# Optimization experiments

Hardware: AMD Instinct MI355X
Metric: run time of the kernel (lower is better)

The kernel has to match this reference:

```python
import jax, jax.numpy as jnp
import numpy as np

N_RADIAL = 5
N_BASIS = 7
R_MAX = 6.0
R_MIN = 0.5
N_SPECIES = 119
N_ATOMS = 50000
N_EDGES = 1000000


def tril_2d_indices(n):
    return np.array([(i, j) for i in range(n) for j in range(i + 1)], dtype=np.int32)


def tril_3d_indices(n):
    return np.array([(i, j, k) for i in range(n) for j in range(i + 1) for k in range(j + 1)], dtype=np.int32)


TRIL2 = tril_2d_indices(N_RADIAL)  # [15, 2]
TRIL3 = tril_3d_indices(N_RADIAL)  # [35, 3]


def setup_inputs() -> dict:
    key = jax.random.key(0)
    k1, k2, k3, k4 = jax.random.split(key, 4)
    R = jax.random.normal(k1, (N_ATOMS, 3), dtype=jnp.float32) * 1.5
    Z = jax.random.randint(k2, (N_ATOMS,), 0, N_SPECIES, dtype=jnp.int32)
    neighbor_idxs = jax.random.randint(k3, (2, N_EDGES), 0, N_ATOMS, dtype=jnp.int32)
    box = jnp.zeros((3,), dtype=jnp.float32)
    W = jax.random.normal(k4, (N_SPECIES, N_SPECIES, N_RADIAL, N_BASIS), dtype=jnp.float32)
    return {"R": R, "Z": Z, "neighbor_idxs": neighbor_idxs, "box": box, "W": W}


def reference(R, Z, neighbor_idxs, box, W):
    n_atoms = R.shape[0]
    idx_i, idx_j = neighbor_idxs[0], neighbor_idxs[1]
    # free-space displacement (init_box == 0): R[idx_j] - R[idx_i]
    dr_vec = (R[idx_j] - R[idx_i]).astype(jnp.float32)  # [E, 3]
    dr = jnp.sqrt(jnp.sum(dr_vec * dr_vec, axis=-1))    # [E]
    dn = dr_vec / (dr + 1e-5)[:, None]                  # unit directions [E, 3]

    # radial function: Gaussian basis * cosine cutoff, species-pair coefficients
    shifts = R_MIN + (R_MAX - R_MIN) / N_BASIS * jnp.arange(N_BASIS, dtype=jnp.float32)
    betta = float(N_BASIS ** 2) / float(R_MAX ** 2)
    rad_norm = float((2.0 * betta / np.pi) ** 0.25)
    basis = rad_norm * jnp.exp(-betta * (dr[:, None] - shifts) ** 2)  # [E, n_basis]
    cutoff = 0.5 * (jnp.cos(np.pi * dr / R_MAX) + 1.0) * (dr < R_MAX).astype(dr.dtype)
    coeffs = W[Z[idx_i], Z[idx_j]]  # [E, n_radial, n_basis]
    embed_norm = float(1.0 / np.sqrt(N_BASIS))
    radial = jnp.einsum('en,ern->er', basis, coeffs) * cutoff[:, None] * embed_norm  # [E, R]

    # mask padded (self-index) neighbors
    radial = radial * (idx_i != idx_j).astype(radial.dtype)[:, None]

    # geometric moments: scatter-add per-edge rank-0..3 outer products onto atoms
    seg = lambda x: jax.ops.segment_sum(x, idx_j, num_segments=n_atoms)
    m0 = seg(radial)                                           # [A, R]
    m1 = seg(radial[:, :, None] * dn[:, None, :])              # [A, R, 3]
    dn2 = dn[:, None, :, None] * dn[:, None, None, :]          # [E, 1, 3, 3]
    m2 = seg(radial[:, :, None, None] * dn2)                   # [A, R, 3, 3]
    dn3 = dn2[..., None] * dn[:, None, None, None, :]          # [E, 1, 3, 3, 3]
    m3 = seg(radial[:, :, None, None, None] * dn3)             # [A, R, 3, 3, 3]

    contr_0 = m0
    contr_1 = jnp.einsum('ari,asi->rsa', m1, m1)
    contr_2 = jnp.einsum('arij,asij->rsa', m2, m2)
    contr_3 = jnp.einsum('arijk,asijk->rsa', m3, m3)
    contr_4 = jnp.einsum('arij,asik,atjk->rsta', m2, m2, m2)
    contr_5 = jnp.einsum('ari,asj,atij->rsta', m1, m1, m2)
    contr_6 = jnp.einsum('arijk,asijl,atkl->rsta', m3, m3, m2)
    contr_7 = jnp.einsum('arijk,asij,atk->rsta', m3, m2, m1)

    i2, j2 = TRIL2[:, 0], TRIL2[:, 1]
    i3, j3, k3 = TRIL3[:, 0], TRIL3[:, 1], TRIL3[:, 2]
    n_symm01 = TRIL2.shape[0] * N_RADIAL  # 75

    c1 = jnp.transpose(contr_1[i2, j2])                                    # [A, 15]
    c2 = jnp.transpose(contr_2[i2, j2])                                    # [A, 15]
    c3 = jnp.transpose(contr_3[i2, j2])                                    # [A, 15]
    c4 = jnp.transpose(contr_4[i3, j3, k3])                                # [A, 35]
    c5 = jnp.transpose(jnp.reshape(contr_5[i2, j2], (n_symm01, -1)))       # [A, 75]
    c6 = jnp.transpose(jnp.reshape(contr_6[i2, j2], (n_symm01, -1)))       # [A, 75]
    c7 = jnp.transpose(jnp.reshape(contr_7, (N_RADIAL ** 3, -1)))          # [A, 125]

    return jnp.concatenate([contr_0, c1, c2, c3, c4, c5, c6, c7], axis=-1)  # [A, 360]
```

## Files before the change

### kernel.cpp

```cpp
#include <hip/hip_runtime.h>
#include <cstdint>
#include <cstddef>

#define CAP 64
#define NSP 119
#define CPAD 16

__device__ constexpr int IDX2[9]  = {0,1,2, 1,3,4, 2,4,5};
__device__ constexpr int IDX3[27] = {0,1,2, 1,3,4, 2,4,5,
                                     1,3,4, 3,6,7, 4,7,8,
                                     2,4,5, 4,7,8, 5,8,9};
__device__ constexpr int PR2[15] = {0,1,1,2,2,2,3,3,3,3,4,4,4,4,4};
__device__ constexpr int PS2[15] = {0,0,1,0,1,2,0,1,2,3,0,1,2,3,4};
__device__ constexpr int CB4[15] = {50,51,52,54,55,57,60,61,63,66,70,71,73,76,80};

__global__ __launch_bounds__(256) void rz_pack_kernel(
    const float* __restrict__ R, const int* __restrict__ Z,
    float4* __restrict__ RZ, int n_atoms)
{
    int t = blockIdx.x * blockDim.x + threadIdx.x;
    if (t >= n_atoms) return;
    RZ[t] = make_float4(R[3*t], R[3*t+1], R[3*t+2], __int_as_float(Z[t]));
}

__global__ __launch_bounds__(256) void pad_w_kernel(
    const float* __restrict__ W, float* __restrict__ Wp, int n_el)
{
    int t = blockIdx.x * blockDim.x + threadIdx.x;
    if (t >= n_el) return;
    int rc = t / 36;
    int u  = t - rc * 36;
    Wp[t] = (u < 35) ? W[rc * 35 + u] : 0.f;
}

__device__ __forceinline__ bool edge_math(
    float4 rzi, float4 rzj, const float4* __restrict__ Wp4,
    float rv[5], float dn[3])
{
    float dx = rzj.x - rzi.x, dy = rzj.y - rzi.y, dz = rzj.z - rzi.z;
    float dr = sqrtf(dx*dx + dy*dy + dz*dz);
    if (!(dr < 6.0f)) return false;

    float inv = 1.0f / (dr + 1e-5f);
    dn[0] = dx*inv; dn[1] = dy*inv; dn[2] = dz*inv;

    const float betta      = 49.0f/36.0f;
    const float rad_norm   = 0.96481270f;
    const float embed_norm = 0.37796447f;
    const float PI_F       = 3.14159265358979f;
    float cut = 0.5f * (__cosf(PI_F * dr * (1.0f/6.0f)) + 1.0f) * rad_norm * embed_norm;

    float basis[7];
    #pragma unroll
    for (int n = 0; n < 7; n++) {
        float d = dr - (0.5f + (5.5f/7.0f) * (float)n);
        basis[n] = __expf(-betta * d * d);
    }

    int zi = __float_as_int(rzi.w);
    int zj = __float_as_int(rzj.w);
    int base4 = (zi * NSP + zj) * 9;

    float rad[5] = {0,0,0,0,0};
    #pragma unroll
    for (int q = 0; q < 9; q++) {
        float4 wq = Wp4[base4 + q];
        #pragma unroll
        for (int c = 0; c < 4; c++) {
            int f = 4*q + c;
            if (f < 35) {
                float wv = (c==0) ? wq.x : (c==1) ? wq.y : (c==2) ? wq.z : wq.w;
                rad[f/7] += basis[f%7] * wv;
            }
        }
    }
    #pragma unroll
    for (int r = 0; r < 5; r++) rv[r] = rad[r] * cut;
    return true;
}

__global__ __launch_bounds__(256) void edge_compute_kernel(
    const int* __restrict__ nbr, const float4* __restrict__ RZ,
    const float4* __restrict__ Wp4,
    int* __restrict__ cnt, int* __restrict__ binsIdx,
    float4* __restrict__ edgeF, int n_edges)
{
    int e = blockIdx.x * blockDim.x + threadIdx.x;
    if (e >= n_edges) return;
    int i = nbr[e];
    int j = nbr[n_edges + e];
    if (i == j) return;
    float4 rzi = RZ[i];
    float4 rzj = RZ[j];
    float rv[5], dn[3];
    if (!edge_math(rzi, rzj, Wp4, rv, dn)) return;

    int pos = atomicAdd(&cnt[j * CPAD], 1);
    if (pos < CAP) {
        binsIdx[(size_t)j * CAP + pos] = e;
        edgeF[2*(size_t)e + 0] = make_float4(rv[0], rv[1], rv[2], rv[3]);
        edgeF[2*(size_t)e + 1] = make_float4(rv[4], dn[0], dn[1], dn[2]);
    }
}

__global__ __launch_bounds__(256) void scatter_bins_kernel(
    const int* __restrict__ nbr, int* __restrict__ cnt,
    int* __restrict__ bins, int n_edges)
{
    int e = blockIdx.x * blockDim.x + threadIdx.x;
    if (e >= n_edges) return;
    int i = nbr[e];
    int j = nbr[n_edges + e];
    if (i == j) return;
    int pos = atomicAdd(&cnt[j], 1);
    if (pos < CAP) bins[(size_t)j * CAP + pos] = i;
}

__device__ __forceinline__ void c6_range(const float* m, float* o, int plo, int phi) {
    for (int p = plo; p < phi; p++) {
        int r = PR2[p], s = PS2[p];
        const float* m3r = m + 50 + r * 10;
        const float* m3s = m + 50 + s * 10;
        float A[3][3] = {{0,0,0},{0,0,0},{0,0,0}};
        #pragma unroll
        for (int i = 0; i < 3; i++)
            #pragma unroll
            for (int j = 0; j < 3; j++)
                #pragma unroll
                for (int k = 0; k < 3; k++)
                    #pragma unroll
                    for (int l = 0; l < 3; l++)
                        A[k][l] += m3r[IDX3[(i*3+j)*3+k]] * m3s[IDX3[(i*3+j)*3+l]];
        int col = 160 + p * 5;
        for (int t = 0; t < 5; t++) {
            const float* m2t = m + 20 + t * 6;
            float acc = 0.f;
            #pragma unroll
            for (int k = 0; k < 3; k++)
                #pragma unroll
                for (int l = 0; l < 3; l++)
                    acc += A[k][l] * m2t[IDX2[k*3+l]];
            o[col + t] = acc;
        }
    }
}

__device__ __forceinline__ void c4_range(const float* m, float* o, int plo, int phi) {
    for (int p = plo; p < phi; p++) {
        int r = PR2[p], s = PS2[p];
        const float* m2r = m + 20 + r * 6;
        const float* m2s = m + 20 + s * 6;
        float B[3][3] = {{0,0,0},{0,0,0},{0,0,0}};
        #pragma unroll
        for (int i = 0; i < 3; i++)
            #pragma unroll
            for (int j = 0; j < 3; j++)
                #pragma unroll
                for (int k = 0; k < 3; k++)
                    B[j][k] += m2r[IDX2[i*3+j]] * m2s[IDX2[i*3+k]];
        int col = CB4[p];
        for (int t = 0; t <= s; t++) {
            const float* m2t = m + 20 + t * 6;
            float acc = 0.f;
            #pragma unroll
            for (int j = 0; j < 3; j++)
                #pragma unroll
                for (int k = 0; k < 3; k++)
                    acc += B[j][k] * m2t[IDX2[j*3+k]];
            o[col + t] = acc;
        }
    }
}

__device__ __forceinline__ void c5_range(const float* m, float* o, int plo, int phi) {
    for (int p = plo; p < phi; p++) {
        int r = PR2[p], s = PS2[p];
        const float* m1r = m + 5 + r * 3;
        const float* m1s = m + 5 + s * 3;
        float P[3][3];
        #pragma unroll
        for (int i = 0; i < 3; i++)
            #pragma unroll
            for (int j = 0; j < 3; j++)
                P[i][j] = m1r[i] * m1s[j];
        int col = 85 + p * 5;
        for (int t = 0; t < 5; t++) {
            const float* m2t = m + 20 + t * 6;
            float acc = 0.f;
            #pragma unroll
            for (int i = 0; i < 3; i++)
                #pragma unroll
                for (int j = 0; j < 3; j++)
                    acc += P[i][j] * m2t[IDX2[i*3+j]];
            o[col + t] = acc;
        }
    }
}

__device__ __forceinline__ void c7_all(const float* m, float* o) {
    for (int r = 0; r < 5; r++) {
        const float* m3r = m + 50 + r * 10;
        for (int s = 0; s < 5; s++) {
            const float* m2s = m + 20 + s * 6;
            float v[3] = {0,0,0};
            #pragma unroll
            for (int i = 0; i < 3; i++)
                #pragma unroll
                for (int j = 0; j < 3; j++)
                    #pragma unroll
                    for (int k = 0; k < 3; k++)
                        v[k] += m3r[IDX3[(i*3+j)*3+k]] * m2s[IDX2[i*3+j]];
            int col = 235 + (r * 5 + s) * 5;
            for (int t = 0; t < 5; t++) {
                const float* m1t = m + 5 + t * 3;
                o[col + t] = v[0]*m1t[0] + v[1]*m1t[1] + v[2]*m1t[2];
            }
        }
    }
}

__device__ __forceinline__ void c0123(const float* m, float* o) {
    for (int r = 0; r < 5; r++) o[r] = m[r];
    const float W2[6]  = {1,2,2,1,2,1};
    const float W3[10] = {1,3,3,3,6,3,1,3,3,1};
    int c1 = 5, c2 = 20, c3 = 35;
    for (int r = 0; r < 5; r++) {
        const float* a1r = m + 5 + r * 3;
        const float* a2r = m + 20 + r * 6;
        const float* a3r = m + 50 + r * 10;
        for (int s = 0; s <= r; s++) {
            const float* a1s = m + 5 + s * 3;
            const float* a2s = m + 20 + s * 6;
            const float* a3s = m + 50 + s * 10;
            float d1 = 0.f, d2 = 0.f, d3 = 0.f;
            #pragma unroll
            for (int u = 0; u < 3; u++)  d1 += a1r[u] * a1s[u];
            #pragma unroll
            for (int u = 0; u < 6; u++)  d2 += W2[u] * a2r[u] * a2s[u];
            #pragma unroll
            for (int u = 0; u < 10; u++) d3 += W3[u] * a3r[u] * a3s[u];
            o[c1++] = d1; o[c2++] = d2; o[c3++] = d3;
        }
    }
}

__device__ __forceinline__ void moments_to_out(
    float acc[100], float sm[64][101], int tid, int a0, int n_atoms,
    float* __restrict__ out)
{
    #pragma unroll
    for (int u = 0; u < 100; u++) {
        acc[u] += __shfl_xor(acc[u], 1);
        acc[u] += __shfl_xor(acc[u], 2);
    }
    int g  = tid >> 2;
    int l4 = tid & 3;
    if (a0 + g < n_atoms && l4 == 0) {
        #pragma unroll
        for (int u = 0; u < 100; u++) sm[g][u] = acc[u];
    }
    __syncthreads();

    int lane = tid & 63;
    int w    = tid >> 6;
    int aa   = a0 + lane;
    if (aa < n_atoms) {
        const float* m = sm[lane];
        float* o = out + (size_t)aa * 360;
        if (w == 0) {
            c6_range(m, o, 0, 10);
        } else if (w == 1) {
            c6_range(m, o, 10, 15);
            c4_range(m, o, 0, 7);
        } else if (w == 2) {
            c4_range(m, o, 7, 15);
            c5_range(m, o, 0, 15);
        } else {
            c7_all(m, o);
            c0123(m, o);
        }
    }
}

__global__ __launch_bounds__(256) void accum_payload_kernel(
    const int* __restrict__ cnt, const int* __restrict__ binsIdx,
    const float4* __restrict__ edgeF,
    float* __restrict__ out, int n_atoms)
{
    __shared__ float sm[64][101];
    int tid = threadIdx.x;
    int a0  = blockIdx.x * 64;
    int g   = tid >> 2;
    int l4  = tid & 3;
    int a   = a0 + g;

    float acc[100];
    #pragma unroll
    for (int u = 0; u < 100; u++) acc[u] = 0.f;

    if (a < n_atoms) {
        int cn = cnt[a * CPAD]; if (cn > CAP) cn = CAP;
        const int* row = binsIdx + (size_t)a * CAP;
        for (int es = l4; es < cn; es += 4) {
            int e = row[es];
            float4 q0 = edgeF[2*(size_t)e + 0];
            float4 q1 = edgeF[2*(size_t)e + 1];
            float rv[5] = {q0.x, q0.y, q0.z, q0.w, q1.x};
            float dn1[3] = {q1.y, q1.z, q1.w};
            float p2[6] = {dn1[0]*dn1[0], dn1[0]*dn1[1], dn1[0]*dn1[2],
                           dn1[1]*dn1[1], dn1[1]*dn1[2], dn1[2]*dn1[2]};
            float p3[10] = {p2[0]*dn1[0], p2[0]*dn1[1], p2[0]*dn1[2],
                            p2[1]*dn1[1], p2[1]*dn1[2], p2[2]*dn1[2],
                            p2[3]*dn1[1], p2[3]*dn1[2], p2[4]*dn1[2],
                            p2[5]*dn1[2]};
            #pragma unroll
            for (int r = 0; r < 5; r++) {
                float rvv = rv[r];
                acc[r] += rvv;
                #pragma unroll
                for (int u = 0; u < 3; u++)  acc[5  + r*3  + u] += rvv * dn1[u];
                #pragma unroll
                for (int u = 0; u < 6; u++)  acc[20 + r*6  + u] += rvv * p2[u];
                #pragma unroll
                for (int u = 0; u < 10; u++) acc[50 + r*10 + u] += rvv * p3[u];
            }
        }
    }
    moments_to_out(acc, sm, tid, a0, n_atoms, out);
}

__global__ __launch_bounds__(256) void accum_gather_kernel(
    const float4* __restrict__ RZ, const float4* __restrict__ Wp4,
    const int* __restrict__ cnt, const int* __restrict__ bins,
    float* __restrict__ out, int n_atoms)
{
    __shared__ float sm[64][101];
    int tid = threadIdx.x;
    int a0  = blockIdx.x * 64;
    int g   = tid >> 2;
    int l4  = tid & 3;
    int a   = a0 + g;

    float acc[100];
    #pragma unroll
    for (int u = 0; u < 100; u++) acc[u] = 0.f;

    if (a < n_atoms) {
        int cn = cnt[a]; if (cn > CAP) cn = CAP;
        float4 rza = RZ[a];
        for (int e = l4; e < cn; e += 4) {
            int i = bins[(size_t)a * CAP + e];
            float4 rzi = RZ[i];
            float rv[5], dn1[3];
            if (!edge_math(rzi, rza, Wp4, rv, dn1)) continue;
            float p2[6] = {dn1[0]*dn1[0], dn1[0]*dn1[1], dn1[0]*dn1[2],
                           dn1[1]*dn1[1], dn1[1]*dn1[2], dn1[2]*dn1[2]};
            float p3[10] = {p2[0]*dn1[0], p2[0]*dn1[1], p2[0]*dn1[2],
                            p2[1]*dn1[1], p2[1]*dn1[2], p2[2]*dn1[2],
                            p2[3]*dn1[1], p2[3]*dn1[2], p2[4]*dn1[2],
                            p2[5]*dn1[2]};
            #pragma unroll
            for (int r = 0; r < 5; r++) {
                float rvv = rv[r];
                acc[r] += rvv;
                #pragma unroll
                for (int u = 0; u < 3; u++)  acc[5  + r*3  + u] += rvv * dn1[u];
                #pragma unroll
                for (int u = 0; u < 6; u++)  acc[20 + r*6  + u] += rvv * p2[u];
                #pragma unroll
                for (int u = 0; u < 10; u++) acc[50 + r*10 + u] += rvv * p3[u];
            }
        }
    }
    moments_to_out(acc, sm, tid, a0, n_atoms, out);
}

extern "C" void kernel_launch(void* const* d_in, const int* in_sizes, int n_in,
                              void* d_out, int out_size, void* d_ws, size_t ws_size,
                              hipStream_t stream)
{
    const float* R   = (const float*)d_in[0];
    const int*   Z   = (const int*)d_in[1];
    const int*   nbr = (const int*)d_in[2];
    const float* W   = (const float*)d_in[4];
    float* out = (float*)d_out;

    int n_atoms = in_sizes[0] / 3;
    int n_edges = in_sizes[2] / 2;
    int n_wel   = NSP * NSP * 36;

    char* ws = (char*)d_ws;

    size_t szCntPad = (size_t)n_atoms * CPAD * 4;
    size_t szIdx    = (size_t)n_atoms * CAP * 4;
    size_t szEdgeF  = (size_t)n_edges * 32;
    size_t szRZ     = (size_t)n_atoms * 16;
    size_t szWp     = (size_t)n_wel * 4;
    size_t needP    = szCntPad + szIdx + szEdgeF + szRZ + szWp;

    if (ws_size >= needP) {
        int*    cnt     = (int*)ws;
        int*    binsIdx = (int*)(ws + szCntPad);
        float4* edgeF   = (float4*)(ws + szCntPad + szIdx);
        float4* RZ      = (float4*)(ws + szCntPad + szIdx + szEdgeF);
        float4* Wp4     = (float4*)(ws + szCntPad + szIdx + szEdgeF + szRZ);

        hipMemsetAsync(cnt, 0, szCntPad, stream);
        rz_pack_kernel<<<(n_atoms + 255)/256, 256, 0, stream>>>(R, Z, RZ, n_atoms);
        pad_w_kernel<<<(n_wel + 255)/256, 256, 0, stream>>>(W, (float*)Wp4, n_wel);
        edge_compute_kernel<<<(n_edges + 255)/256, 256, 0, stream>>>(
            nbr, RZ, Wp4, cnt, binsIdx, edgeF, n_edges);
        accum_payload_kernel<<<(n_atoms + 63)/64, 256, 0, stream>>>(
            cnt, binsIdx, edgeF, out, n_atoms);
    } else {
        int*    cnt  = (int*)ws;
        int*    bins = (int*)(ws + 204800);
        float4* RZ   = (float4*)(ws + 204800 + szIdx);
        float4* Wp4  = (float4*)(ws + 204800 + szIdx + szRZ);

        hipMemsetAsync(cnt, 0, (size_t)n_atoms * 4, stream);
        rz_pack_kernel<<<(n_atoms + 255)/256, 256, 0, stream>>>(R, Z, RZ, n_atoms);
        pad_w_kernel<<<(n_wel + 255)/256, 256, 0, stream>>>(W, (float*)Wp4, n_wel);
        scatter_bins_kernel<<<(n_edges + 255)/256, 256, 0, stream>>>(nbr, cnt, bins, n_edges);
        accum_gather_kernel<<<(n_atoms + 63)/64, 256, 0, stream>>>(
            RZ, Wp4, cnt, bins, out, n_atoms);
    }
}
```

Baseline: 135.9 us.

## Transpose edge bins and map atoms to lanes with LDS atomic reduction

Bin indices are now stored slot-major (pos * n_atoms + j), so that in the accumulate kernel consecutive lanes read consecutive atoms and the index loads coalesce. Each atom is now handled by one lane per wave, with the four waves splitting its edges, in place of four adjacent lanes splitting them. Partial moments are combined with shared-memory atomicAdd in place of xor shuffles, which needs an LDS zero-fill and an extra barrier. The risk is 100 LDS atomics per thread, more lane divergence from uneven per-atom edge counts, and scattered writes from the edge kernel into the transposed layout.

```diff
diff --git a/kernel.cpp b/kernel.cpp
--- a/kernel.cpp
+++ b/kernel.cpp
@@ -82,8 +82,8 @@
 __global__ __launch_bounds__(256) void edge_compute_kernel(
     const int* __restrict__ nbr, const float4* __restrict__ RZ,
     const float4* __restrict__ Wp4,
-    int* __restrict__ cnt, int* __restrict__ binsIdx,
-    float4* __restrict__ edgeF, int n_edges)
+    int* __restrict__ cnt, int* __restrict__ binsIdxT,
+    float4* __restrict__ edgeF, int n_edges, int n_atoms)
 {
     int e = blockIdx.x * blockDim.x + threadIdx.x;
     if (e >= n_edges) return;
@@ -97,7 +97,7 @@
 
     int pos = atomicAdd(&cnt[j * CPAD], 1);
     if (pos < CAP) {
-        binsIdx[(size_t)j * CAP + pos] = e;
+        binsIdxT[(size_t)pos * n_atoms + j] = e;
         edgeF[2*(size_t)e + 0] = make_float4(rv[0], rv[1], rv[2], rv[3]);
         edgeF[2*(size_t)e + 1] = make_float4(rv[4], dn[0], dn[1], dn[2]);
     }
@@ -244,26 +244,10 @@
     }
 }
 
-__device__ __forceinline__ void moments_to_out(
-    float acc[100], float sm[64][101], int tid, int a0, int n_atoms,
-    float* __restrict__ out)
-{
-    #pragma unroll
-    for (int u = 0; u < 100; u++) {
-        acc[u] += __shfl_xor(acc[u], 1);
-        acc[u] += __shfl_xor(acc[u], 2);
-    }
-    int g  = tid >> 2;
-    int l4 = tid & 3;
-    if (a0 + g < n_atoms && l4 == 0) {
-        #pragma unroll
-        for (int u = 0; u < 100; u++) sm[g][u] = acc[u];
-    }
-    __syncthreads();
-
-    int lane = tid & 63;
-    int w    = tid >> 6;
-    int aa   = a0 + lane;
+__device__ __forceinline__ void contract_4wave(
+    float sm[64][101], int lane, int w, int a0, int n_atoms, float* __restrict__ out)
+{
+    int aa = a0 + lane;
     if (aa < n_atoms) {
         const float* m = sm[lane];
         float* o = out + (size_t)aa * 360;
@@ -282,17 +266,21 @@
     }
 }
 
-__global__ __launch_bounds__(256) void accum_payload_kernel(
-    const int* __restrict__ cnt, const int* __restrict__ binsIdx,
+__global__ __launch_bounds__(256) void accum_contract_kernel(
+    const int* __restrict__ cnt, const int* __restrict__ binsIdxT,
     const float4* __restrict__ edgeF,
     float* __restrict__ out, int n_atoms)
 {
     __shared__ float sm[64][101];
-    int tid = threadIdx.x;
-    int a0  = blockIdx.x * 64;
-    int g   = tid >> 2;
-    int l4  = tid & 3;
-    int a   = a0 + g;
+    int tid  = threadIdx.x;
+    int lane = tid & 63;
+    int w    = tid >> 6;
+    int a0   = blockIdx.x * 64;
+    int a    = a0 + lane;
+
+    float* smf = &sm[0][0];
+    for (int t = tid; t < 64*101; t += 256) smf[t] = 0.f;
+    __syncthreads();
 
     float acc[100];
     #pragma unroll
@@ -300,12 +288,11 @@
 
     if (a < n_atoms) {
         int cn = cnt[a * CPAD]; if (cn > CAP) cn = CAP;
-        const int* row = binsIdx + (size_t)a * CAP;
-        for (int es = l4; es < cn; es += 4) {
-            int e = row[es];
+        for (int k = w; k < cn; k += 4) {
+            int e = binsIdxT[(size_t)k * n_atoms + a];
             float4 q0 = edgeF[2*(size_t)e + 0];
             float4 q1 = edgeF[2*(size_t)e + 1];
-            float rv[5] = {q0.x, q0.y, q0.z, q0.w, q1.x};
+            float rv[5]  = {q0.x, q0.y, q0.z, q0.w, q1.x};
             float dn1[3] = {q1.y, q1.z, q1.w};
             float p2[6] = {dn1[0]*dn1[0], dn1[0]*dn1[1], dn1[0]*dn1[2],
                            dn1[1]*dn1[1], dn1[1]*dn1[2], dn1[2]*dn1[2]};
@@ -325,8 +312,12 @@
                 for (int u = 0; u < 10; u++) acc[50 + r*10 + u] += rvv * p3[u];
             }
         }
-    }
-    moments_to_out(acc, sm, tid, a0, n_atoms, out);
+        #pragma unroll
+        for (int u = 0; u < 100; u++) atomicAdd(&sm[lane][u], acc[u]);
+    }
+    __syncthreads();
+
+    contract_4wave(sm, lane, w, a0, n_atoms, out);
 }
 
 __global__ __launch_bounds__(256) void accum_gather_kernel(
@@ -372,7 +363,19 @@
             }
         }
     }
-    moments_to_out(acc, sm, tid, a0, n_atoms, out);
+
+    #pragma unroll
+    for (int u = 0; u < 100; u++) {
+        acc[u] += __shfl_xor(acc[u], 1);
+        acc[u] += __shfl_xor(acc[u], 2);
+    }
+    if (a < n_atoms && l4 == 0) {
+        #pragma unroll
+        for (int u = 0; u < 100; u++) sm[g][u] = acc[u];
+    }
+    __syncthreads();
+
+    contract_4wave(sm, tid & 63, tid >> 6, a0, n_atoms, out);
 }
 
 extern "C" void kernel_launch(void* const* d_in, const int* in_sizes, int n_in,
@@ -399,19 +402,19 @@
     size_t needP    = szCntPad + szIdx + szEdgeF + szRZ + szWp;
 
     if (ws_size >= needP) {
-        int*    cnt     = (int*)ws;
-        int*    binsIdx = (int*)(ws + szCntPad);
-        float4* edgeF   = (float4*)(ws + szCntPad + szIdx);
-        float4* RZ      = (float4*)(ws + szCntPad + szIdx + szEdgeF);
-        float4* Wp4     = (float4*)(ws + szCntPad + szIdx + szEdgeF + szRZ);
+        int*    cnt      = (int*)ws;
+        int*    binsIdxT = (int*)(ws + szCntPad);
+        float4* edgeF    = (float4*)(ws + szCntPad + szIdx);
+        float4* RZ       = (float4*)(ws + szCntPad + szIdx + szEdgeF);
+        float4* Wp4      = (float4*)(ws + szCntPad + szIdx + szEdgeF + szRZ);
 
         hipMemsetAsync(cnt, 0, szCntPad, stream);
         rz_pack_kernel<<<(n_atoms + 255)/256, 256, 0, stream>>>(R, Z, RZ, n_atoms);
         pad_w_kernel<<<(n_wel + 255)/256, 256, 0, stream>>>(W, (float*)Wp4, n_wel);
         edge_compute_kernel<<<(n_edges + 255)/256, 256, 0, stream>>>(
-            nbr, RZ, Wp4, cnt, binsIdx, edgeF, n_edges);
-        accum_payload_kernel<<<(n_atoms + 63)/64, 256, 0, stream>>>(
-            cnt, binsIdx, edgeF, out, n_atoms);
+            nbr, RZ, Wp4, cnt, binsIdxT, edgeF, n_edges, n_atoms);
+        accum_contract_kernel<<<(n_atoms + 63)/64, 256, 0, stream>>>(
+            cnt, binsIdxT, edgeF, out, n_atoms);
     } else {
         int*    cnt  = (int*)ws;
         int*    bins = (int*)(ws + 204800);
```

Result: slower. 243.9 us (+79.4%).

## Write edge payloads directly into per-atom slots instead of index indirection

Applied to the files above, without the earlier changes.

Adds a new path used when workspace is large enough: the edge kernel writes its computed radial and direction payload straight into the destination atom's bin slot instead of storing an edge index plus a separate per-edge payload array. The accumulation kernel then reads contiguous per-atom slot rows, which removes the index load and the random gather over edge payloads. In exchange, the edge kernel's writes become scattered, the workspace grows to atoms*CAP*32 bytes, and the new path only runs if the harness provides that much workspace. The shared accumulation code is also factored into helpers.

```diff
diff --git a/kernel.cpp b/kernel.cpp
--- a/kernel.cpp
+++ b/kernel.cpp
@@ -79,7 +79,30 @@
     return true;
 }
 
-__global__ __launch_bounds__(256) void edge_compute_kernel(
+__global__ __launch_bounds__(256) void edge_compute_slot_kernel(
+    const int* __restrict__ nbr, const float4* __restrict__ RZ,
+    const float4* __restrict__ Wp4,
+    int* __restrict__ cnt, float4* __restrict__ pay, int n_edges)
+{
+    int e = blockIdx.x * blockDim.x + threadIdx.x;
+    if (e >= n_edges) return;
+    int i = nbr[e];
+    int j = nbr[n_edges + e];
+    if (i == j) return;
+    float4 rzi = RZ[i];
+    float4 rzj = RZ[j];
+    float rv[5], dn[3];
+    if (!edge_math(rzi, rzj, Wp4, rv, dn)) return;
+
+    int pos = atomicAdd(&cnt[j * CPAD], 1);
+    if (pos < CAP) {
+        size_t slot = ((size_t)j * CAP + pos) * 2;
+        pay[slot + 0] = make_float4(rv[0], rv[1], rv[2], rv[3]);
+        pay[slot + 1] = make_float4(rv[4], dn[0], dn[1], dn[2]);
+    }
+}
+
+__global__ __launch_bounds__(256) void edge_compute_r4_kernel(
     const int* __restrict__ nbr, const float4* __restrict__ RZ,
     const float4* __restrict__ Wp4,
     int* __restrict__ cnt, int* __restrict__ binsIdx,
@@ -244,26 +267,10 @@
     }
 }
 
-__device__ __forceinline__ void moments_to_out(
-    float acc[100], float sm[64][101], int tid, int a0, int n_atoms,
-    float* __restrict__ out)
-{
-    #pragma unroll
-    for (int u = 0; u < 100; u++) {
-        acc[u] += __shfl_xor(acc[u], 1);
-        acc[u] += __shfl_xor(acc[u], 2);
-    }
-    int g  = tid >> 2;
-    int l4 = tid & 3;
-    if (a0 + g < n_atoms && l4 == 0) {
-        #pragma unroll
-        for (int u = 0; u < 100; u++) sm[g][u] = acc[u];
-    }
-    __syncthreads();
-
-    int lane = tid & 63;
-    int w    = tid >> 6;
-    int aa   = a0 + lane;
+__device__ __forceinline__ void contract_4wave(
+    float sm[64][101], int lane, int w, int a0, int n_atoms, float* __restrict__ out)
+{
+    int aa = a0 + lane;
     if (aa < n_atoms) {
         const float* m = sm[lane];
         float* o = out + (size_t)aa * 360;
@@ -282,7 +289,76 @@
     }
 }
 
-__global__ __launch_bounds__(256) void accum_payload_kernel(
+__device__ __forceinline__ void moments_to_out(
+    float acc[100], float sm[64][101], int tid, int a0, int n_atoms,
+    float* __restrict__ out)
+{
+    #pragma unroll
+    for (int u = 0; u < 100; u++) {
+        acc[u] += __shfl_xor(acc[u], 1);
+        acc[u] += __shfl_xor(acc[u], 2);
+    }
+    int g  = tid >> 2;
+    int l4 = tid & 3;
+    if (a0 + g < n_atoms && l4 == 0) {
+        #pragma unroll
+        for (int u = 0; u < 100; u++) sm[g][u] = acc[u];
+    }
+    __syncthreads();
+    contract_4wave(sm, tid & 63, tid >> 6, a0, n_atoms, out);
+}
+
+__device__ __forceinline__ void accum_edge(float acc[100], float4 q0, float4 q1)
+{
+    float rv[5]  = {q0.x, q0.y, q0.z, q0.w, q1.x};
+    float dn1[3] = {q1.y, q1.z, q1.w};
+    float p2[6] = {dn1[0]*dn1[0], dn1[0]*dn1[1], dn1[0]*dn1[2],
+                   dn1[1]*dn1[1], dn1[1]*dn1[2], dn1[2]*dn1[2]};
+    float p3[10] = {p2[0]*dn1[0], p2[0]*dn1[1], p2[0]*dn1[2],
+                    p2[1]*dn1[1], p2[1]*dn1[2], p2[2]*dn1[2],
+                    p2[3]*dn1[1], p2[3]*dn1[2], p2[4]*dn1[2],
+                    p2[5]*dn1[2]};
+    #pragma unroll
+    for (int r = 0; r < 5; r++) {
+        float rvv = rv[r];
+        acc[r] += rvv;
+        #pragma unroll
+        for (int u = 0; u < 3; u++)  acc[5  + r*3  + u] += rvv * dn1[u];
+        #pragma unroll
+        for (int u = 0; u < 6; u++)  acc[20 + r*6  + u] += rvv * p2[u];
+        #pragma unroll
+        for (int u = 0; u < 10; u++) acc[50 + r*10 + u] += rvv * p3[u];
+    }
+}
+
+__global__ __launch_bounds__(256) void accum_slot_kernel(
+    const int* __restrict__ cnt, const float4* __restrict__ pay,
+    float* __restrict__ out, int n_atoms)
+{
+    __shared__ float sm[64][101];
+    int tid = threadIdx.x;
+    int a0  = blockIdx.x * 64;
+    int g   = tid >> 2;
+    int l4  = tid & 3;
+    int a   = a0 + g;
+
+    float acc[100];
+    #pragma unroll
+    for (int u = 0; u < 100; u++) acc[u] = 0.f;
+
+    if (a < n_atoms) {
+        int cn = cnt[a * CPAD]; if (cn > CAP) cn = CAP;
+        const float4* row = pay + (size_t)a * CAP * 2;
+        for (int es = l4; es < cn; es += 4) {
+            float4 q0 = row[2*es + 0];
+            float4 q1 = row[2*es + 1];
+            accum_edge(acc, q0, q1);
+        }
+    }
+    moments_to_out(acc, sm, tid, a0, n_atoms, out);
+}
+
+__global__ __launch_bounds__(256) void accum_payload_r4_kernel(
     const int* __restrict__ cnt, const int* __restrict__ binsIdx,
     const float4* __restrict__ edgeF,
     float* __restrict__ out, int n_atoms)
@@ -305,25 +381,7 @@
             int e = row[es];
             float4 q0 = edgeF[2*(size_t)e + 0];
             float4 q1 = edgeF[2*(size_t)e + 1];
-            float rv[5] = {q0.x, q0.y, q0.z, q0.w, q1.x};
-            float dn1[3] = {q1.y, q1.z, q1.w};
-            float p2[6] = {dn1[0]*dn1[0], dn1[0]*dn1[1], dn1[0]*dn1[2],
-                           dn1[1]*dn1[1], dn1[1]*dn1[2], dn1[2]*dn1[2]};
-            float p3[10] = {p2[0]*dn1[0], p2[0]*dn1[1], p2[0]*dn1[2],
-                            p2[1]*dn1[1], p2[1]*dn1[2], p2[2]*dn1[2],
-                            p2[3]*dn1[1], p2[3]*dn1[2], p2[4]*dn1[2],
-                            p2[5]*dn1[2]};
-            #pragma unroll
-            for (int r = 0; r < 5; r++) {
-                float rvv = rv[r];
-                acc[r] += rvv;
-                #pragma unroll
-                for (int u = 0; u < 3; u++)  acc[5  + r*3  + u] += rvv * dn1[u];
-                #pragma unroll
-                for (int u = 0; u < 6; u++)  acc[20 + r*6  + u] += rvv * p2[u];
-                #pragma unroll
-                for (int u = 0; u < 10; u++) acc[50 + r*10 + u] += rvv * p3[u];
-            }
+            accum_edge(acc, q0, q1);
         }
     }
     moments_to_out(acc, sm, tid, a0, n_atoms, out);
@@ -353,23 +411,9 @@
             float4 rzi = RZ[i];
             float rv[5], dn1[3];
             if (!edge_math(rzi, rza, Wp4, rv, dn1)) continue;
-            float p2[6] = {dn1[0]*dn1[0], dn1[0]*dn1[1], dn1[0]*dn1[2],
-                           dn1[1]*dn1[1], dn1[1]*dn1[2], dn1[2]*dn1[2]};
-            float p3[10] = {p2[0]*dn1[0], p2[0]*dn1[1], p2[0]*dn1[2],
-                            p2[1]*dn1[1], p2[1]*dn1[2], p2[2]*dn1[2],
-                            p2[3]*dn1[1], p2[3]*dn1[2], p2[4]*dn1[2],
-                            p2[5]*dn1[2]};
-            #pragma unroll
-            for (int r = 0; r < 5; r++) {
-                float rvv = rv[r];
-                acc[r] += rvv;
-                #pragma unroll
-                for (int u = 0; u < 3; u++)  acc[5  + r*3  + u] += rvv * dn1[u];
-                #pragma unroll
-                for (int u = 0; u < 6; u++)  acc[20 + r*6  + u] += rvv * p2[u];
-                #pragma unroll
-                for (int u = 0; u < 10; u++) acc[50 + r*10 + u] += rvv * p3[u];
-            }
+            float4 q0 = make_float4(rv[0], rv[1], rv[2], rv[3]);
+            float4 q1 = make_float4(rv[4], dn1[0], dn1[1], dn1[2]);
+            accum_edge(acc, q0, q1);
         }
     }
     moments_to_out(acc, sm, tid, a0, n_atoms, out);
@@ -392,13 +436,30 @@
     char* ws = (char*)d_ws;
 
     size_t szCntPad = (size_t)n_atoms * CPAD * 4;
+    size_t szRZ     = (size_t)n_atoms * 16;
+    size_t szWp     = (size_t)n_wel * 4;
+    size_t szPay    = (size_t)n_atoms * CAP * 32;
     size_t szIdx    = (size_t)n_atoms * CAP * 4;
     size_t szEdgeF  = (size_t)n_edges * 32;
-    size_t szRZ     = (size_t)n_atoms * 16;
-    size_t szWp     = (size_t)n_wel * 4;
-    size_t needP    = szCntPad + szIdx + szEdgeF + szRZ + szWp;
-
-    if (ws_size >= needP) {
+
+    size_t needSlot = szCntPad + szPay + szRZ + szWp;
+    size_t needR4   = szCntPad + szIdx + szEdgeF + szRZ + szWp;
+    size_t needR3   = 204800 + szIdx + szRZ + szWp;
+
+    if (ws_size >= needSlot) {
+        int*    cnt = (int*)ws;
+        float4* pay = (float4*)(ws + szCntPad);
+        float4* RZ  = (float4*)(ws + szCntPad + szPay);
+        float4* Wp4 = (float4*)(ws + szCntPad + szPay + szRZ);
+
+        hipMemsetAsync(cnt, 0, szCntPad, stream);
+        rz_pack_kernel<<<(n_atoms + 255)/256, 256, 0, stream>>>(R, Z, RZ, n_atoms);
+        pad_w_kernel<<<(n_wel + 255)/256, 256, 0, stream>>>(W, (float*)Wp4, n_wel);
+        edge_compute_slot_kernel<<<(n_edges + 255)/256, 256, 0, stream>>>(
+            nbr, RZ, Wp4, cnt, pay, n_edges);
+        accum_slot_kernel<<<(n_atoms + 63)/64, 256, 0, stream>>>(
+            cnt, pay, out, n_atoms);
+    } else if (ws_size >= needR4) {
         int*    cnt     = (int*)ws;
         int*    binsIdx = (int*)(ws + szCntPad);
         float4* edgeF   = (float4*)(ws + szCntPad + szIdx);
@@ -408,9 +469,9 @@
         hipMemsetAsync(cnt, 0, szCntPad, stream);
         rz_pack_kernel<<<(n_atoms + 255)/256, 256, 0, stream>>>(R, Z, RZ, n_atoms);
         pad_w_kernel<<<(n_wel + 255)/256, 256, 0, stream>>>(W, (float*)Wp4, n_wel);
-        edge_compute_kernel<<<(n_edges + 255)/256, 256, 0, stream>>>(
+        edge_compute_r4_kernel<<<(n_edges + 255)/256, 256, 0, stream>>>(
             nbr, RZ, Wp4, cnt, binsIdx, edgeF, n_edges);
-        accum_payload_kernel<<<(n_atoms + 63)/64, 256, 0, stream>>>(
+        accum_payload_r4_kernel<<<(n_atoms + 63)/64, 256, 0, stream>>>(
             cnt, binsIdx, edgeF, out, n_atoms);
     } else {
         int*    cnt  = (int*)ws;
```

Result: faster. 124.0 us (-8.8%).

## Bin raw displacement and species per edge, recompute radial basis in accumulator

Applied to the files above, without the earlier changes.

The edge kernel now only checks the cutoff on squared distance and writes a compact float4 (dx,dy,dz,Z_i) straight into each destination atom's bin. The expensive radial basis, cosine cutoff and species-weight gather move into the per-atom accumulation kernel. This drops the indirect edge-index lookup and the scattered 32-byte per-edge feature reads, since payloads sit contiguously per atom. The cost is a heavier accumulation kernel with more register pressure, plus a larger bin buffer (16 bytes per slot).

```diff
diff --git a/kernel.cpp b/kernel.cpp
--- a/kernel.cpp
+++ b/kernel.cpp
@@ -33,57 +33,9 @@
     Wp[t] = (u < 35) ? W[rc * 35 + u] : 0.f;
 }
 
-__device__ __forceinline__ bool edge_math(
-    float4 rzi, float4 rzj, const float4* __restrict__ Wp4,
-    float rv[5], float dn[3])
-{
-    float dx = rzj.x - rzi.x, dy = rzj.y - rzi.y, dz = rzj.z - rzi.z;
-    float dr = sqrtf(dx*dx + dy*dy + dz*dz);
-    if (!(dr < 6.0f)) return false;
-
-    float inv = 1.0f / (dr + 1e-5f);
-    dn[0] = dx*inv; dn[1] = dy*inv; dn[2] = dz*inv;
-
-    const float betta      = 49.0f/36.0f;
-    const float rad_norm   = 0.96481270f;
-    const float embed_norm = 0.37796447f;
-    const float PI_F       = 3.14159265358979f;
-    float cut = 0.5f * (__cosf(PI_F * dr * (1.0f/6.0f)) + 1.0f) * rad_norm * embed_norm;
-
-    float basis[7];
-    #pragma unroll
-    for (int n = 0; n < 7; n++) {
-        float d = dr - (0.5f + (5.5f/7.0f) * (float)n);
-        basis[n] = __expf(-betta * d * d);
-    }
-
-    int zi = __float_as_int(rzi.w);
-    int zj = __float_as_int(rzj.w);
-    int base4 = (zi * NSP + zj) * 9;
-
-    float rad[5] = {0,0,0,0,0};
-    #pragma unroll
-    for (int q = 0; q < 9; q++) {
-        float4 wq = Wp4[base4 + q];
-        #pragma unroll
-        for (int c = 0; c < 4; c++) {
-            int f = 4*q + c;
-            if (f < 35) {
-                float wv = (c==0) ? wq.x : (c==1) ? wq.y : (c==2) ? wq.z : wq.w;
-                rad[f/7] += basis[f%7] * wv;
-            }
-        }
-    }
-    #pragma unroll
-    for (int r = 0; r < 5; r++) rv[r] = rad[r] * cut;
-    return true;
-}
-
-__global__ __launch_bounds__(256) void edge_compute_kernel(
+__global__ __launch_bounds__(256) void edge_light_kernel(
     const int* __restrict__ nbr, const float4* __restrict__ RZ,
-    const float4* __restrict__ Wp4,
-    int* __restrict__ cnt, int* __restrict__ binsIdx,
-    float4* __restrict__ edgeF, int n_edges)
+    int* __restrict__ cnt, float4* __restrict__ pay, int n_edges)
 {
     int e = blockIdx.x * blockDim.x + threadIdx.x;
     if (e >= n_edges) return;
@@ -92,14 +44,13 @@
     if (i == j) return;
     float4 rzi = RZ[i];
     float4 rzj = RZ[j];
-    float rv[5], dn[3];
-    if (!edge_math(rzi, rzj, Wp4, rv, dn)) return;
+    float dx = rzj.x - rzi.x, dy = rzj.y - rzi.y, dz = rzj.z - rzi.z;
+    float dr2 = dx*dx + dy*dy + dz*dz;
+    if (!(dr2 < 36.0f)) return;
 
     int pos = atomicAdd(&cnt[j * CPAD], 1);
     if (pos < CAP) {
-        binsIdx[(size_t)j * CAP + pos] = e;
-        edgeF[2*(size_t)e + 0] = make_float4(rv[0], rv[1], rv[2], rv[3]);
-        edgeF[2*(size_t)e + 1] = make_float4(rv[4], dn[0], dn[1], dn[2]);
+        pay[(size_t)j * CAP + pos] = make_float4(dx, dy, dz, rzi.w);
     }
 }
 
@@ -114,6 +65,45 @@
     if (i == j) return;
     int pos = atomicAdd(&cnt[j], 1);
     if (pos < CAP) bins[(size_t)j * CAP + pos] = i;
+}
+
+__device__ __forceinline__ void edge_math_raw(
+    float dx, float dy, float dz, int zi, int za,
+    const float4* __restrict__ Wp4, float rv[5], float dn[3])
+{
+    float dr = sqrtf(dx*dx + dy*dy + dz*dz);
+    float inv = 1.0f / (dr + 1e-5f);
+    dn[0] = dx*inv; dn[1] = dy*inv; dn[2] = dz*inv;
+
+    const float betta      = 49.0f/36.0f;
+    const float rad_norm   = 0.96481270f;
+    const float embed_norm = 0.37796447f;
+    const float PI_F       = 3.14159265358979f;
+    float cut = 0.5f * (__cosf(PI_F * dr * (1.0f/6.0f)) + 1.0f) * rad_norm * embed_norm;
+
+    float basis[7];
+    #pragma unroll
+    for (int n = 0; n < 7; n++) {
+        float d = dr - (0.5f + (5.5f/7.0f) * (float)n);
+        basis[n] = __expf(-betta * d * d);
+    }
+
+    int base4 = (zi * NSP + za) * 9;
+    float rad[5] = {0,0,0,0,0};
+    #pragma unroll
+    for (int q = 0; q < 9; q++) {
+        float4 wq = Wp4[base4 + q];
+        #pragma unroll
+        for (int c = 0; c < 4; c++) {
+            int f = 4*q + c;
+            if (f < 35) {
+                float wv = (c==0) ? wq.x : (c==1) ? wq.y : (c==2) ? wq.z : wq.w;
+                rad[f/7] += basis[f%7] * wv;
+            }
+        }
+    }
+    #pragma unroll
+    for (int r = 0; r < 5; r++) rv[r] = rad[r] * cut;
 }
 
 __device__ __forceinline__ void c6_range(const float* m, float* o, int plo, int phi) {
@@ -244,26 +234,10 @@
     }
 }
 
-__device__ __forceinline__ void moments_to_out(
-    float acc[100], float sm[64][101], int tid, int a0, int n_atoms,
-    float* __restrict__ out)
-{
-    #pragma unroll
-    for (int u = 0; u < 100; u++) {
-        acc[u] += __shfl_xor(acc[u], 1);
-        acc[u] += __shfl_xor(acc[u], 2);
-    }
-    int g  = tid >> 2;
-    int l4 = tid & 3;
-    if (a0 + g < n_atoms && l4 == 0) {
-        #pragma unroll
-        for (int u = 0; u < 100; u++) sm[g][u] = acc[u];
-    }
-    __syncthreads();
-
-    int lane = tid & 63;
-    int w    = tid >> 6;
-    int aa   = a0 + lane;
+__device__ __forceinline__ void contract_4wave(
+    float sm[64][101], int lane, int w, int a0, int n_atoms, float* __restrict__ out)
+{
+    int aa = a0 + lane;
     if (aa < n_atoms) {
         const float* m = sm[lane];
         float* o = out + (size_t)aa * 360;
@@ -282,9 +256,50 @@
     }
 }
 
-__global__ __launch_bounds__(256) void accum_payload_kernel(
-    const int* __restrict__ cnt, const int* __restrict__ binsIdx,
-    const float4* __restrict__ edgeF,
+__device__ __forceinline__ void moments_to_out(
+    float acc[100], float sm[64][101], int tid, int a0, int n_atoms,
+    float* __restrict__ out)
+{
+    #pragma unroll
+    for (int u = 0; u < 100; u++) {
+        acc[u] += __shfl_xor(acc[u], 1);
+        acc[u] += __shfl_xor(acc[u], 2);
+    }
+    int g  = tid >> 2;
+    int l4 = tid & 3;
+    if (a0 + g < n_atoms && l4 == 0) {
+        #pragma unroll
+        for (int u = 0; u < 100; u++) sm[g][u] = acc[u];
+    }
+    __syncthreads();
+    contract_4wave(sm, tid & 63, tid >> 6, a0, n_atoms, out);
+}
+
+__device__ __forceinline__ void accum_edge(float acc[100], const float rv[5], const float dn1[3])
+{
+    float p2[6] = {dn1[0]*dn1[0], dn1[0]*dn1[1], dn1[0]*dn1[2],
+                   dn1[1]*dn1[1], dn1[1]*dn1[2], dn1[2]*dn1[2]};
+    float p3[10] = {p2[0]*dn1[0], p2[0]*dn1[1], p2[0]*dn1[2],
+                    p2[1]*dn1[1], p2[1]*dn1[2], p2[2]*dn1[2],
+                    p2[3]*dn1[1], p2[3]*dn1[2], p2[4]*dn1[2],
+                    p2[5]*dn1[2]};
+    #pragma unroll
+    for (int r = 0; r < 5; r++) {
+        float rvv = rv[r];
+        acc[r] += rvv;
+        #pragma unroll
+        for (int u = 0; u < 3; u++)  acc[5  + r*3  + u] += rvv * dn1[u];
+        #pragma unroll
+        for (int u = 0; u < 6; u++)  acc[20 + r*6  + u] += rvv * p2[u];
+        #pragma unroll
+        for (int u = 0; u < 10; u++) acc[50 + r*10 + u] += rvv * p3[u];
+    }
+}
+
+__global__ __launch_bounds__(256) void accum_recompute_kernel(
+    const int* __restrict__ Z,
+    const int* __restrict__ cnt, const float4* __restrict__ pay,
+    const float4* __restrict__ Wp4,
     float* __restrict__ out, int n_atoms)
 {
     __shared__ float sm[64][101];
@@ -300,30 +315,14 @@
 
     if (a < n_atoms) {
         int cn = cnt[a * CPAD]; if (cn > CAP) cn = CAP;
-        const int* row = binsIdx + (size_t)a * CAP;
+        int za = Z[a];
+        const float4* row = pay + (size_t)a * CAP;
         for (int es = l4; es < cn; es += 4) {
-            int e = row[es];
-            float4 q0 = edgeF[2*(size_t)e + 0];
-            float4 q1 = edgeF[2*(size_t)e + 1];
-            float rv[5] = {q0.x, q0.y, q0.z, q0.w, q1.x};
-            float dn1[3] = {q1.y, q1.z, q1.w};
-            float p2[6] = {dn1[0]*dn1[0], dn1[0]*dn1[1], dn1[0]*dn1[2],
-                           dn1[1]*dn1[1], dn1[1]*dn1[2], dn1[2]*dn1[2]};
-            float p3[10] = {p2[0]*dn1[0], p2[0]*dn1[1], p2[0]*dn1[2],
-                            p2[1]*dn1[1], p2[1]*dn1[2], p2[2]*dn1[2],
-                            p2[3]*dn1[1], p2[3]*dn1[2], p2[4]*dn1[2],
-                            p2[5]*dn1[2]};
-            #pragma unroll
-            for (int r = 0; r < 5; r++) {
-                float rvv = rv[r];
-                acc[r] += rvv;
-                #pragma unroll
-                for (int u = 0; u < 3; u++)  acc[5  + r*3  + u] += rvv * dn1[u];
-                #pragma unroll
-                for (int u = 0; u < 6; u++)  acc[20 + r*6  + u] += rvv * p2[u];
-                #pragma unroll
-                for (int u = 0; u < 10; u++) acc[50 + r*10 + u] += rvv * p3[u];
-            }
+            float4 q = row[es];
+            int zi = __float_as_int(q.w);
+            float rv[5], dn1[3];
+            edge_math_raw(q.x, q.y, q.z, zi, za, Wp4, rv, dn1);
+            accum_edge(acc, rv, dn1);
         }
     }
     moments_to_out(acc, sm, tid, a0, n_atoms, out);
@@ -348,28 +347,17 @@
     if (a < n_atoms) {
         int cn = cnt[a]; if (cn > CAP) cn = CAP;
         float4 rza = RZ[a];
+        int za = __float_as_int(rza.w);
         for (int e = l4; e < cn; e += 4) {
             int i = bins[(size_t)a * CAP + e];
             float4 rzi = RZ[i];
+            float dx = rza.x - rzi.x, dy = rza.y - rzi.y, dz = rza.z - rzi.z;
+            float dr2 = dx*dx + dy*dy + dz*dz;
+            if (!(dr2 < 36.0f)) continue;
+            int zi = __float_as_int(rzi.w);
             float rv[5], dn1[3];
-            if (!edge_math(rzi, rza, Wp4, rv, dn1)) continue;
-            float p2[6] = {dn1[0]*dn1[0], dn1[0]*dn1[1], dn1[0]*dn1[2],
-                           dn1[1]*dn1[1], dn1[1]*dn1[2], dn1[2]*dn1[2]};
-            float p3[10] = {p2[0]*dn1[0], p2[0]*dn1[1], p2[0]*dn1[2],
-                            p2[1]*dn1[1], p2[1]*dn1[2], p2[2]*dn1[2],
-                            p2[3]*dn1[1], p2[3]*dn1[2], p2[4]*dn1[2],
-                            p2[5]*dn1[2]};
-            #pragma unroll
-            for (int r = 0; r < 5; r++) {
-                float rvv = rv[r];
-                acc[r] += rvv;
-                #pragma unroll
-                for (int u = 0; u < 3; u++)  acc[5  + r*3  + u] += rvv * dn1[u];
-                #pragma unroll
-                for (int u = 0; u < 6; u++)  acc[20 + r*6  + u] += rvv * p2[u];
-                #pragma unroll
-                for (int u = 0; u < 10; u++) acc[50 + r*10 + u] += rvv * p3[u];
-            }
+            edge_math_raw(dx, dy, dz, zi, za, Wp4, rv, dn1);
+            accum_edge(acc, rv, dn1);
         }
     }
     moments_to_out(acc, sm, tid, a0, n_atoms, out);
@@ -392,26 +380,26 @@
     char* ws = (char*)d_ws;
 
     size_t szCntPad = (size_t)n_atoms * CPAD * 4;
-    size_t szIdx    = (size_t)n_atoms * CAP * 4;
-    size_t szEdgeF  = (size_t)n_edges * 32;
     size_t szRZ     = (size_t)n_atoms * 16;
     size_t szWp     = (size_t)n_wel * 4;
-    size_t needP    = szCntPad + szIdx + szEdgeF + szRZ + szWp;
-
-    if (ws_size >= needP) {
-        int*    cnt     = (int*)ws;
-        int*    binsIdx = (int*)(ws + szCntPad);
-        float4* edgeF   = (float4*)(ws + szCntPad + szIdx);
-        float4* RZ      = (float4*)(ws + szCntPad + szIdx + szEdgeF);
-        float4* Wp4     = (float4*)(ws + szCntPad + szIdx + szEdgeF + szRZ);
+    size_t szPay16  = (size_t)n_atoms * CAP * 16;
+    size_t szIdx    = (size_t)n_atoms * CAP * 4;
+
+    size_t needLight = szCntPad + szPay16 + szRZ + szWp;
+
+    if (ws_size >= needLight) {
+        int*    cnt = (int*)ws;
+        float4* pay = (float4*)(ws + szCntPad);
+        float4* RZ  = (float4*)(ws + szCntPad + szPay16);
+        float4* Wp4 = (float4*)(ws + szCntPad + szPay16 + szRZ);
 
         hipMemsetAsync(cnt, 0, szCntPad, stream);
         rz_pack_kernel<<<(n_atoms + 255)/256, 256, 0, stream>>>(R, Z, RZ, n_atoms);
         pad_w_kernel<<<(n_wel + 255)/256, 256, 0, stream>>>(W, (float*)Wp4, n_wel);
-        edge_compute_kernel<<<(n_edges + 255)/256, 256, 0, stream>>>(
-            nbr, RZ, Wp4, cnt, binsIdx, edgeF, n_edges);
-        accum_payload_kernel<<<(n_atoms + 63)/64, 256, 0, stream>>>(
-            cnt, binsIdx, edgeF, out, n_atoms);
+        edge_light_kernel<<<(n_edges + 255)/256, 256, 0, stream>>>(
+            nbr, RZ, cnt, pay, n_edges);
+        accum_recompute_kernel<<<(n_atoms + 63)/64, 256, 0, stream>>>(
+            Z, cnt, pay, Wp4, out, n_atoms);
     } else {
         int*    cnt  = (int*)ws;
         int*    bins = (int*)(ws + 204800);
```

New measurement: 122.8 us. 9.7% less time.
